# Kernel tuning notes

Measured on AMD Instinct MI355X. Metric: run time of the kernel, lower is better.

Reference implementation:

```python
import jax, jax.numpy as jnp
import numpy as np

R3D = (0.1, 0.2, 0.4)
R6D = (0.15, 0.25, 0.45)
K = 64  # max_num_neighbors in radius()


def setup_inputs() -> dict:
    key = jax.random.key(0)
    k1, k2, k3, k4 = jax.random.split(key, 4)
    B, M = 8, 2048
    pos = jax.random.uniform(k1, (B, M, 3), dtype=jnp.float32)        # points in unit cube
    x = 0.05 * jax.random.normal(k2, (B, M, 3), dtype=jnp.float32)    # predicted coords/features
    w = 0.5 * jax.random.normal(k3, (1, len(R3D)), dtype=jnp.float32)  # lin1.weight [1, S]
    b = 0.1 * jax.random.normal(k4, (1,), dtype=jnp.float32)           # lin1.bias [1]
    return {"x": x, "pos": pos, "w": w, "b": b}


def _radius_knn(P, r, k=K):
    # P: [B, M, D]. Returns (idx, mask): k nearest neighbors per point (incl. self)
    # and a mask of those actually within radius r (== torch_cluster.radius with
    # max_num_neighbors=k, deterministic nearest-first selection).
    sq = jnp.sum(P * P, axis=-1)                                   # [B, M]
    d2 = sq[:, :, None] + sq[:, None, :] - 2.0 * jnp.einsum('bmd,bnd->bmn', P, P)
    neg_vals, idx = jax.lax.top_k(-d2, k)                          # k smallest distances
    mask = (-neg_vals) <= r * r                                    # [B, M, k]
    return idx, mask


def _gather(v, idx):
    # v: [B, M, D], idx: [B, M, k] -> [B, M, k, D]
    B = v.shape[0]
    return v[jnp.arange(B)[:, None, None], idx]


def reference(x, pos, w, b):
    B, M, _ = x.shape
    pos_ext = jnp.concatenate([pos, x], axis=-1)                   # [B, M, 6]
    msgs = []
    for r3, r6 in zip(R3D, R6D):
        # 6D radius graph -> scatter_mean of x over neighbors
        idx6, m6 = _radius_knn(pos_ext, r6)                        # [B, M, K]
        xs = _gather(x, idx6)                                      # [B, M, K, 3]
        cnt6 = jnp.sum(m6, axis=-1).astype(x.dtype)                # >=1 (self edge)
        x_centers = jnp.sum(xs * m6[..., None], axis=2) / cnt6[..., None]  # [B, M, 3]
        # 3D radius graph -> mean of ||x_centers_i - x_centers_j|| per node
        idx3, m3 = _radius_knn(pos, r3)                            # [B, M, K]
        diff = x_centers[:, :, None, :] - _gather(x_centers, idx3)  # [B, M, K, 3]
        s = jnp.sum(diff * diff, axis=-1)
        d = jnp.sqrt(jnp.maximum(s, 1e-12))                        # safe norm (grad at 0)
        cnt3 = jnp.sum(m3, axis=-1).astype(x.dtype)
        msgs.append(jnp.sum(d * m3, axis=-1) / cnt3)               # [B, M]
    msg = jnp.stack(msgs, axis=-1)                                 # [B, M, S]
    conf = jax.nn.sigmoid(jnp.einsum('bms,os->bmo', msg, w) + b)   # [B, M, 1]
    return conf[..., 0].reshape(B * M)                             # flat [N], like conf[:, 0]
```

## Files before the change

kernel.cpp:

```cpp
#include <hip/hip_runtime.h>
#include <hip/hip_fp16.h>
#include <math.h>

#define MPTS 2048
#define NBATCH 8
#define NT 32
#define KMAX 64
#define NBIN 128
#define BCAP 24
#define TPB 512

typedef unsigned short u16;
typedef unsigned int u32;
typedef unsigned long long u64;

static __device__ __forceinline__ int mbcnt64(u64 m) {
  return __builtin_amdgcn_mbcnt_hi((u32)(m >> 32),
                                   __builtin_amdgcn_mbcnt_lo((u32)m, 0));
}

static __device__ __forceinline__ u32 packh2(float a, float b) {
  __half2 h = __floats2half2_rn(a, b);
  return *reinterpret_cast<u32*>(&h);
}
static __device__ __forceinline__ float2 unpackh2(u32 w) {
  __half2 h = *reinterpret_cast<__half2*>(&w);
  return __half22float2(h);
}

template <bool COMPACT>
__global__ __launch_bounds__(TPB, 8) void kernelA(
    const float* __restrict__ x, const float* __restrict__ pos,
    float4* __restrict__ xci, float* __restrict__ tau3, u16* __restrict__ nbr) {
  __shared__ __align__(16) float4 P4[MPTS];
  __shared__ __align__(16) u32 XH[MPTS];
  __shared__ __align__(16) u32 histAll[8 * NBIN];

  const int tid  = threadIdx.x;
  const int wv   = tid >> 6;
  const int lane = tid & 63;
  const int pt   = wv >> 1;
  const int mtr  = wv & 1;
  const int wid  = blockIdx.x * 4 + pt;
  const int b    = wid >> 11;
  const int i    = wid & (MPTS - 1);
  const float* posb = pos + b * MPTS * 3;
  const float* xb   = x   + b * MPTS * 3;

  for (int p = tid; p < MPTS; p += TPB) {
    P4[p] = make_float4(posb[3*p+0], posb[3*p+1], posb[3*p+2], xb[3*p+0]);
    XH[p] = packh2(xb[3*p+1], xb[3*p+2]);
  }
  ((uint2*)histAll)[tid] = make_uint2(0u, 0u);
  __syncthreads();

  u32* hw = &histAll[wv * NBIN];

  const float4 pi4 = P4[i];
  const float2 xi2 = unpackh2(XH[i]);
  const float2 c0 = make_float2(pi4.x, pi4.y);
  const float2 c1 = make_float2(pi4.z, pi4.w);
  const float2 c2 = xi2;

  const float R2 = mtr ? 0.2025f : 0.16f;
  const float SC = mtr ? (128.0f / 0.2025f) : (128.0f / 0.16f);

  float da[NT];
  if (mtr == 0) {
#pragma unroll
    for (int k = 0; k < NT; ++k) {
      const int j = k * 64 + lane;
      const float4 pj = P4[j];
      const float2 d01 = make_float2(pj.x, pj.y) - c0;
      const float dz = pj.z - pi4.z;
      const float2 sq = d01 * d01;
      const float a = sq.x + sq.y + dz * dz;
      da[k] = a;
      const int bb = (int)(a * (128.0f / 0.16f));
      if ((u32)bb < 128u) atomicAdd(&hw[bb], 1u);
    }
  } else {
#pragma unroll
    for (int k = 0; k < NT; ++k) {
      const int j = k * 64 + lane;
      const float4 pj = P4[j];
      const float2 xj = unpackh2(XH[j]);
      const float2 a0 = make_float2(pj.x, pj.y) - c0;
      const float2 a1 = make_float2(pj.z, pj.w) - c1;
      const float2 a2 = xj - c2;
      float2 s = a0 * a0;
      s += a1 * a1;
      s += a2 * a2;
      const float a = s.x + s.y;
      da[k] = a;
      const int bb = (int)(a * (128.0f / 0.2025f));
      if ((u32)bb < 128u) atomicAdd(&hw[bb], 1u);
    }
  }

  const u32 h0 = hw[2*lane], h1 = hw[2*lane+1];
  const u32 s2 = h0 + h1;
  u32 incl = s2;
#pragma unroll
  for (int off = 1; off < 64; off <<= 1) {
    const u32 tt = __shfl_up(incl, off, 64);
    if (lane >= off) incl += tt;
  }
  const u32 tot = __shfl(incl, 63, 64);
  float t = R2;

  if (tot > 64u) {
    const u32 excl = incl - s2;
    const u64 m = __ballot((excl < 64u) && (incl >= 64u));
    const int L = __builtin_ctzll(m);
    const u32 c0b = __shfl(excl, L, 64);
    const u32 g0 = __shfl(h0, L, 64);
    const u32 g1 = __shfl(h1, L, 64);
    int B; u32 cb, n;
    if (c0b + g0 >= 64u) { B = 2*L;     cb = c0b;      n = g0; }
    else                 { B = 2*L + 1; cb = c0b + g0; n = g1; }

    if (lane == 0) hw[0] = 0u;
    float* bv = (float*)&hw[1];

#pragma unroll
    for (int k = 0; k < NT; ++k) {
      const int bb = (int)(da[k] * SC);
      if (bb == B) {
        const u32 s = atomicAdd(&hw[0], 1u);
        if (s < (u32)BCAP) bv[s] = da[k];
      }
    }

    if (n <= (u32)BCAP) {
      const int nn = (int)n;
      const float v = (lane < nn) ? bv[lane] : 3.0e38f;
      u32 rank = 0;
      for (int cc = 0; cc < nn; ++cc) {
        const float w = __shfl(v, cc, 64);
        rank += ((w < v) || (w == v && cc < lane)) ? 1u : 0u;
      }
      const u64 sm = __ballot((lane < nn) && (rank == (u32)(63 - (int)cb)));
      t = __shfl(v, __builtin_ctzll(sm), 64);
    } else {
      float lo = (float)B * (R2 / (float)NBIN), hi = lo + R2 / (float)NBIN;
      for (int it = 0; it < 26; ++it) {
        const float mid = 0.5f * (lo + hi);
        int c = 0;
#pragma unroll
        for (int k = 0; k < NT; ++k) c += __popcll(__ballot(da[k] <= mid));
        if (c >= 64) { hi = mid; if (c == 64) break; } else lo = mid;
      }
      t = hi;
    }
  }

  u16* lw = (u16*)&hw[1 + BCAP];
  const float q0 = mtr ? 0.0225f : 0.01f;
  const float q1 = mtr ? 0.0625f : 0.04f;
  int base = 0;
#pragma unroll
  for (int k = 0; k < NT; ++k) {
    const int j = k * 64 + lane;
    const bool sel = (da[k] <= t);
    const u64 m = __ballot(sel);
    const int s = base + mbcnt64(m);
    if (sel && s < KMAX) {
      const int cl = (da[k] > q0) + (da[k] > q1);
      lw[s] = (u16)(j | (cl << 11));
    }
    base += __popcll(m);
  }
  const int cn = base < KMAX ? base : KMAX;

  if (mtr == 0) {
    if (COMPACT)
      nbr[(size_t)wid * KMAX + lane] = (lane < cn) ? lw[lane] : (u16)(3u << 11);
    if (lane == 0) tau3[wid] = t;
  } else {
    const u16 e = (lane < cn) ? lw[lane] : (u16)0xFFFF;
    const int cl = (e >> 11) & 3;
    const int jj = e & (MPTS - 1);
    const float xjx = P4[jj].w;
    const float2 xj = unpackh2(XH[jj]);
    const bool v2 = (cl <= 2), v1 = (cl <= 1), v0 = (cl == 0);

    float2 v2a[6];
    v2a[0] = v0 ? make_float2(xjx, xj.x) : make_float2(0.f, 0.f);
    v2a[1] = v0 ? make_float2(xj.y, 1.f) : make_float2(0.f, 0.f);
    v2a[2] = v1 ? make_float2(xjx, xj.x) : make_float2(0.f, 0.f);
    v2a[3] = v1 ? make_float2(xj.y, 1.f) : make_float2(0.f, 0.f);
    v2a[4] = v2 ? make_float2(xjx, xj.x) : make_float2(0.f, 0.f);
    v2a[5] = v2 ? make_float2(xj.y, 1.f) : make_float2(0.f, 0.f);

#pragma unroll
    for (int v = 0; v < 6; ++v)
#pragma unroll
      for (int off = 32; off > 0; off >>= 1) {
        float2 o;
        o.x = __shfl_xor(v2a[v].x, off, 64);
        o.y = __shfl_xor(v2a[v].y, off, 64);
        v2a[v] += o;
      }

    if (lane == 0) {
#pragma unroll
      for (int s = 0; s < 3; ++s) {
        const float inv = 1.f / v2a[2*s+1].y;
        xci[(size_t)wid * 3 + s] =
            make_float4(v2a[2*s].x * inv, v2a[2*s].y * inv, v2a[2*s+1].x * inv, 0.f);
      }
    }
  }
}

__global__ __launch_bounds__(256) void kernelB_fast(
    const float4* __restrict__ xci, const float* __restrict__ wlin,
    const float* __restrict__ blin, const u16* __restrict__ nbr,
    float* __restrict__ out) {
  const int wid  = (blockIdx.x * 256 + threadIdx.x) >> 6;
  const int lane = threadIdx.x & 63;
  const int pbase = wid & ~(MPTS - 1);

  const u16 e = nbr[(size_t)wid * KMAX + lane];
  const int cl = e >> 11;
  const int gj = pbase + (e & (MPTS - 1));

  const float4 ci0 = xci[(size_t)wid*3 + 0];
  const float4 ci1 = xci[(size_t)wid*3 + 1];
  const float4 ci2 = xci[(size_t)wid*3 + 2];

  float s0 = 0.f, s1 = 0.f, s2 = 0.f, n0 = 0.f, n1 = 0.f, n2 = 0.f;
  if (cl <= 2) {
    const float4 cj2 = xci[(size_t)gj*3 + 2];
    float ux = ci2.x - cj2.x, uy = ci2.y - cj2.y, uz = ci2.z - cj2.z;
    s2 = sqrtf(fmaxf(ux*ux + uy*uy + uz*uz, 1e-12f)); n2 = 1.f;
    if (cl <= 1) {
      const float4 cj1 = xci[(size_t)gj*3 + 1];
      ux = ci1.x - cj1.x; uy = ci1.y - cj1.y; uz = ci1.z - cj1.z;
      s1 = sqrtf(fmaxf(ux*ux + uy*uy + uz*uz, 1e-12f)); n1 = 1.f;
      if (cl == 0) {
        const float4 cj0 = xci[(size_t)gj*3 + 0];
        ux = ci0.x - cj0.x; uy = ci0.y - cj0.y; uz = ci0.z - cj0.z;
        s0 = sqrtf(fmaxf(ux*ux + uy*uy + uz*uz, 1e-12f)); n0 = 1.f;
      }
    }
  }

  float vals[6] = {s0, s1, s2, n0, n1, n2};
#pragma unroll
  for (int v = 0; v < 6; ++v)
#pragma unroll
    for (int off = 32; off > 0; off >>= 1)
      vals[v] += __shfl_xor(vals[v], off, 64);

  if (lane == 0) {
    const float msg0 = vals[0] / vals[3];
    const float msg1 = vals[1] / vals[4];
    const float msg2 = vals[2] / vals[5];
    const float z = wlin[0]*msg0 + wlin[1]*msg1 + wlin[2]*msg2 + blin[0];
    out[wid] = 1.f / (1.f + expf(-z));
  }
}

__global__ __launch_bounds__(256) void kernelB_slow(
    const float* __restrict__ pos, const float* __restrict__ wlin,
    const float* __restrict__ blin, const float4* __restrict__ xci,
    const float* __restrict__ tau3, float* __restrict__ out) {
  const int wid  = (blockIdx.x * 256 + threadIdx.x) >> 6;
  const int lane = threadIdx.x & 63;
  const int b = wid >> 11;
  const int i = wid & (MPTS - 1);
  const float* posb = pos + b * MPTS * 3;
  const int pbase = b * MPTS;

  const float pix = posb[3*i+0], piy = posb[3*i+1], piz = posb[3*i+2];
  const float t3 = tau3[wid];
  const float thr0 = fminf(0.01f, t3);
  const float thr1 = fminf(0.04f, t3);

  const float4 ci0 = xci[(size_t)wid*3 + 0];
  const float4 ci1 = xci[(size_t)wid*3 + 1];
  const float4 ci2 = xci[(size_t)wid*3 + 2];

  float s0=0.f, s1=0.f, s2=0.f, n0=0.f, n1=0.f, n2=0.f;
  for (int k = 0; k < NT; ++k) {
    const int j = k * 64 + lane;
    const float dx = posb[3*j+0] - pix;
    const float dy = posb[3*j+1] - piy;
    const float dz = posb[3*j+2] - piz;
    const float a3 = dx*dx + dy*dy + dz*dz;
    if (a3 <= t3) {
      const float4 cj2 = xci[(size_t)(pbase + j)*3 + 2];
      float ux = ci2.x-cj2.x, uy = ci2.y-cj2.y, uz = ci2.z-cj2.z;
      s2 += sqrtf(fmaxf(ux*ux+uy*uy+uz*uz, 1e-12f)); n2 += 1.f;
      if (a3 <= thr1) {
        const float4 cj1 = xci[(size_t)(pbase + j)*3 + 1];
        ux = ci1.x-cj1.x; uy = ci1.y-cj1.y; uz = ci1.z-cj1.z;
        s1 += sqrtf(fmaxf(ux*ux+uy*uy+uz*uz, 1e-12f)); n1 += 1.f;
        if (a3 <= thr0) {
          const float4 cj0 = xci[(size_t)(pbase + j)*3 + 0];
          ux = ci0.x-cj0.x; uy = ci0.y-cj0.y; uz = ci0.z-cj0.z;
          s0 += sqrtf(fmaxf(ux*ux+uy*uy+uz*uz, 1e-12f)); n0 += 1.f;
        }
      }
    }
  }

  float vals[6] = {s0, s1, s2, n0, n1, n2};
#pragma unroll
  for (int v = 0; v < 6; ++v)
#pragma unroll
    for (int off = 32; off > 0; off >>= 1)
      vals[v] += __shfl_xor(vals[v], off, 64);

  if (lane == 0) {
    const float msg0 = vals[0] / vals[3];
    const float msg1 = vals[1] / vals[4];
    const float msg2 = vals[2] / vals[5];
    const float z = wlin[0]*msg0 + wlin[1]*msg1 + wlin[2]*msg2 + blin[0];
    out[wid] = 1.f / (1.f + expf(-z));
  }
}

extern "C" void kernel_launch(void* const* d_in, const int* in_sizes, int n_in,
                              void* d_out, int out_size, void* d_ws, size_t ws_size,
                              hipStream_t stream) {
  (void)in_sizes; (void)n_in; (void)out_size;
  const float* x    = (const float*)d_in[0];
  const float* pos  = (const float*)d_in[1];
  const float* wlin = (const float*)d_in[2];
  const float* blin = (const float*)d_in[3];
  float* out = (float*)d_out;

  const size_t npts = (size_t)NBATCH * MPTS;
  const size_t xci_bytes = npts * 3 * sizeof(float4);
  const size_t tau_bytes = npts * sizeof(float);
  const size_t nbr_bytes = npts * KMAX * sizeof(u16);
  float4* xci = (float4*)d_ws;
  float* tau3 = (float*)((char*)d_ws + xci_bytes);
  u16* nbr    = (u16*)((char*)d_ws + xci_bytes + tau_bytes);
  const bool fast = ws_size >= xci_bytes + tau_bytes + nbr_bytes;

  const int nblocksA = (int)(npts / 4);
  const int nblocksB = (int)(npts * 64 / 256);
  if (fast) {
    kernelA<true><<<nblocksA, TPB, 0, stream>>>(x, pos, xci, tau3, nbr);
    kernelB_fast<<<nblocksB, 256, 0, stream>>>(xci, wlin, blin, nbr, out);
  } else {
    kernelA<false><<<nblocksA, TPB, 0, stream>>>(x, pos, xci, tau3, nbr);
    kernelB_slow<<<nblocksB, 256, 0, stream>>>(pos, wlin, blin, xci, tau3, out);
  }
}
```

Before: 85.30 us.

## Quantize neighbor distances to 16-bit and pack two per register

Squared distances are stored as 16-bit quantized integers packed in pairs, which halves the per-lane register array and may raise occupancy. The bin-refinement binary search is replaced by an integer threshold: exact rank selection on quantized values, or the bin's upper edge when the bin overflows. Radius classification and tau3 now work on quantized values, so near-threshold ties and overflow cases can pick slightly different neighbor sets than the float version.

```diff
diff --git a/kernel.cpp b/kernel.cpp
--- a/kernel.cpp
+++ b/kernel.cpp
@@ -26,6 +26,11 @@
 static __device__ __forceinline__ float2 unpackh2(u32 w) {
   __half2 h = *reinterpret_cast<__half2*>(&w);
   return __half22float2(h);
+}
+
+static __device__ __forceinline__ u32 quantd(float a, float sc16) {
+  const int qi = (int)(a * sc16);
+  return (u32)(qi > 65535 ? 65535 : qi);
 }
 
 template <bool COMPACT>
@@ -62,39 +67,47 @@
   const float2 c1 = make_float2(pi4.z, pi4.w);
   const float2 c2 = xi2;
 
-  const float R2 = mtr ? 0.2025f : 0.16f;
-  const float SC = mtr ? (128.0f / 0.2025f) : (128.0f / 0.16f);
-
-  float da[NT];
+  const float SC3 = 65534.0f / 0.16f;
+  const float SC6 = 65534.0f / 0.2025f;
+
+  u32 dq[NT / 2];
   if (mtr == 0) {
 #pragma unroll
-    for (int k = 0; k < NT; ++k) {
-      const int j = k * 64 + lane;
-      const float4 pj = P4[j];
-      const float2 d01 = make_float2(pj.x, pj.y) - c0;
-      const float dz = pj.z - pi4.z;
-      const float2 sq = d01 * d01;
-      const float a = sq.x + sq.y + dz * dz;
-      da[k] = a;
-      const int bb = (int)(a * (128.0f / 0.16f));
-      if ((u32)bb < 128u) atomicAdd(&hw[bb], 1u);
+    for (int k2 = 0; k2 < NT / 2; ++k2) {
+      const int j = (2 * k2) * 64 + lane;
+      const float4 pa = P4[j];
+      const float4 pb = P4[j + 64];
+      const float2 e0 = make_float2(pa.x, pa.y) - c0;
+      const float2 e1 = make_float2(pb.x, pb.y) - c0;
+      const float dza = pa.z - pi4.z, dzb = pb.z - pi4.z;
+      const float2 s0 = e0 * e0, s1 = e1 * e1;
+      const float a0 = s0.x + s0.y + dza * dza;
+      const float a1 = s1.x + s1.y + dzb * dzb;
+      const u32 q0 = quantd(a0, SC3), q1 = quantd(a1, SC3);
+      dq[k2] = q0 | (q1 << 16);
+      if (q0 < 65535u) atomicAdd(&hw[q0 >> 9], 1u);
+      if (q1 < 65535u) atomicAdd(&hw[q1 >> 9], 1u);
     }
   } else {
 #pragma unroll
-    for (int k = 0; k < NT; ++k) {
-      const int j = k * 64 + lane;
-      const float4 pj = P4[j];
-      const float2 xj = unpackh2(XH[j]);
-      const float2 a0 = make_float2(pj.x, pj.y) - c0;
-      const float2 a1 = make_float2(pj.z, pj.w) - c1;
-      const float2 a2 = xj - c2;
-      float2 s = a0 * a0;
-      s += a1 * a1;
-      s += a2 * a2;
-      const float a = s.x + s.y;
-      da[k] = a;
-      const int bb = (int)(a * (128.0f / 0.2025f));
-      if ((u32)bb < 128u) atomicAdd(&hw[bb], 1u);
+    for (int k2 = 0; k2 < NT / 2; ++k2) {
+      const int j = (2 * k2) * 64 + lane;
+      const float4 pa = P4[j];
+      const float4 pb = P4[j + 64];
+      const float2 xa = unpackh2(XH[j]);
+      const float2 xcb = unpackh2(XH[j + 64]);
+      const float2 a00 = make_float2(pa.x, pa.y) - c0;
+      const float2 a01 = make_float2(pa.z, pa.w) - c1;
+      const float2 a02 = xa - c2;
+      float2 sa = a00 * a00; sa += a01 * a01; sa += a02 * a02;
+      const float2 b00 = make_float2(pb.x, pb.y) - c0;
+      const float2 b01 = make_float2(pb.z, pb.w) - c1;
+      const float2 b02 = xcb - c2;
+      float2 sb = b00 * b00; sb += b01 * b01; sb += b02 * b02;
+      const u32 q0 = quantd(sa.x + sa.y, SC6), q1 = quantd(sb.x + sb.y, SC6);
+      dq[k2] = q0 | (q1 << 16);
+      if (q0 < 65535u) atomicAdd(&hw[q0 >> 9], 1u);
+      if (q1 < 65535u) atomicAdd(&hw[q1 >> 9], 1u);
     }
   }
 
@@ -107,7 +120,7 @@
     if (lane >= off) incl += tt;
   }
   const u32 tot = __shfl(incl, 63, 64);
-  float t = R2;
+  u32 qt = 65534u;
 
   if (tot > 64u) {
     const u32 excl = incl - s2;
@@ -121,62 +134,72 @@
     else                 { B = 2*L + 1; cb = c0b + g0; n = g1; }
 
     if (lane == 0) hw[0] = 0u;
-    float* bv = (float*)&hw[1];
-
-#pragma unroll
-    for (int k = 0; k < NT; ++k) {
-      const int bb = (int)(da[k] * SC);
-      if (bb == B) {
+    u32* bv = &hw[1];
+
+#pragma unroll
+    for (int k2 = 0; k2 < NT / 2; ++k2) {
+      const u32 q0 = dq[k2] & 0xFFFFu, q1 = dq[k2] >> 16;
+      if (q0 < 65535u && (int)(q0 >> 9) == B) {
         const u32 s = atomicAdd(&hw[0], 1u);
-        if (s < (u32)BCAP) bv[s] = da[k];
+        if (s < (u32)BCAP) bv[s] = q0;
+      }
+      if (q1 < 65535u && (int)(q1 >> 9) == B) {
+        const u32 s = atomicAdd(&hw[0], 1u);
+        if (s < (u32)BCAP) bv[s] = q1;
       }
     }
 
     if (n <= (u32)BCAP) {
       const int nn = (int)n;
-      const float v = (lane < nn) ? bv[lane] : 3.0e38f;
+      const u32 v = (lane < nn) ? bv[lane] : 0xFFFFFFFFu;
       u32 rank = 0;
       for (int cc = 0; cc < nn; ++cc) {
-        const float w = __shfl(v, cc, 64);
+        const u32 w = __shfl(v, cc, 64);
         rank += ((w < v) || (w == v && cc < lane)) ? 1u : 0u;
       }
       const u64 sm = __ballot((lane < nn) && (rank == (u32)(63 - (int)cb)));
-      t = __shfl(v, __builtin_ctzll(sm), 64);
+      qt = __shfl(v, __builtin_ctzll(sm), 64);
     } else {
-      float lo = (float)B * (R2 / (float)NBIN), hi = lo + R2 / (float)NBIN;
-      for (int it = 0; it < 26; ++it) {
-        const float mid = 0.5f * (lo + hi);
-        int c = 0;
-#pragma unroll
-        for (int k = 0; k < NT; ++k) c += __popcll(__ballot(da[k] <= mid));
-        if (c >= 64) { hi = mid; if (c == 64) break; } else lo = mid;
-      }
-      t = hi;
+      qt = (u32)((B << 9) + 511);
     }
   }
 
   u16* lw = (u16*)&hw[1 + BCAP];
-  const float q0 = mtr ? 0.0225f : 0.01f;
-  const float q1 = mtr ? 0.0625f : 0.04f;
+  const u32 qr0 = mtr ? 7281u : 4095u;
+  const u32 qr1 = mtr ? 20226u : 16383u;
   int base = 0;
 #pragma unroll
-  for (int k = 0; k < NT; ++k) {
-    const int j = k * 64 + lane;
-    const bool sel = (da[k] <= t);
-    const u64 m = __ballot(sel);
-    const int s = base + mbcnt64(m);
-    if (sel && s < KMAX) {
-      const int cl = (da[k] > q0) + (da[k] > q1);
-      lw[s] = (u16)(j | (cl << 11));
-    }
-    base += __popcll(m);
+  for (int k2 = 0; k2 < NT / 2; ++k2) {
+    const u32 q0 = dq[k2] & 0xFFFFu, q1 = dq[k2] >> 16;
+    {
+      const int j = (2 * k2) * 64 + lane;
+      const bool sel = (q0 <= qt);
+      const u64 m = __ballot(sel);
+      const int s = base + mbcnt64(m);
+      if (sel && s < KMAX) {
+        const int cl = (q0 > qr0) + (q0 > qr1);
+        lw[s] = (u16)(j | (cl << 11));
+      }
+      base += __popcll(m);
+    }
+    {
+      const int j = (2 * k2 + 1) * 64 + lane;
+      const bool sel = (q1 <= qt);
+      const u64 m = __ballot(sel);
+      const int s = base + mbcnt64(m);
+      if (sel && s < KMAX) {
+        const int cl = (q1 > qr0) + (q1 > qr1);
+        lw[s] = (u16)(j | (cl << 11));
+      }
+      base += __popcll(m);
+    }
   }
   const int cn = base < KMAX ? base : KMAX;
 
   if (mtr == 0) {
     if (COMPACT)
       nbr[(size_t)wid * KMAX + lane] = (lane < cn) ? lw[lane] : (u16)(3u << 11);
-    if (lane == 0) tau3[wid] = t;
+    if (lane == 0) tau3[wid] = ((float)qt + 1.0f) * (0.16f / 65534.0f);
   } else {
     const u16 e = (lane < cn) ? lw[lane] : (u16)0xFFFF;
     const int cl = (e >> 11) & 3;
```

Result: slower. 87.38 us (+2.4%).
